# Kernel tuning notes

Hardware: AMD Instinct MI355X
Metric: run time of the kernel (lower is better)

## Reference

```python
import jax, jax.numpy as jnp
from jax import lax
import numpy as np

EPSILON = 22.6  # Cech radius; ~mean pairwise distance of N(0,1) points in 256-d


def _betti1(x, eps):
    """Faithful port of compute_betti_number for one epsilon. x: (B,T,C)."""
    B, T, C = x.shape
    # pairwise squared distances; compare d2 < eps^2 == (dist < eps), avoids sqrt
    sq = jnp.sum(x * x, axis=-1)                                  # (B,T)
    d2 = sq[:, :, None] + sq[:, None, :] - 2.0 * jnp.einsum('btc,bsc->bts', x, x)
    adj = d2 < (eps * eps)                                        # (B,T,T) bool; diagonal True (dist 0 < eps), matching torch
    adj = lax.stop_gradient(adj)                                  # original detaches x before topology
    # original: n_edges = np.sum(adjacency) // 2, diagonal included
    n_edges = jnp.sum(adj, axis=(1, 2)).astype(jnp.int32) // 2    # (B,)
    # connected components via min-label propagation + pointer jumping
    labels0 = jnp.broadcast_to(jnp.arange(T, dtype=jnp.int32), (B, T))

    def cond(state):
        return state[1]

    def body(state):
        labels, _ = state
        # min label among neighbors (diag True includes self)
        prop = jnp.min(jnp.where(adj, labels[:, None, :], T), axis=2).astype(jnp.int32)
        new = jnp.minimum(labels, prop)
        new = jnp.take_along_axis(new, new, axis=1)               # pointer jump -> O(log) convergence
        return new, jnp.any(new != labels)

    labels, _ = lax.while_loop(cond, body, (labels0, jnp.array(True)))
    # converged label = min index in component -> count roots
    n_comp = jnp.sum(labels == jnp.arange(T, dtype=jnp.int32)[None, :], axis=1).astype(jnp.int32)
    betti1 = jnp.maximum(0, n_edges - T + n_comp)                 # max(0, E - V + C)
    return betti1


def reference(x_before, x_after):
    betti_before = _betti1(x_before, EPSILON)
    betti_after = _betti1(x_after, EPSILON)
    diff = betti_after.astype(jnp.float32) - betti_before.astype(jnp.float32)
    return jnp.mean(diff * diff)


def setup_inputs() -> dict:
    key = jax.random.key(0)
    k1, k2 = jax.random.split(key)
    B, T, C = 4, 4096, 256
    x_before = jax.random.normal(k1, (B, T, C), dtype=jnp.float32)
    x_after = jax.random.normal(k2, (B, T, C), dtype=jnp.float32)
    return {"x_before": x_before, "x_after": x_after}
```

## Files before the change

kernel.cpp:

```cpp
#include <hip/hip_runtime.h>
#include <stdint.h>

#define TDIM 4096
#define CDIM 256
#define NMAT 8

typedef __attribute__((ext_vector_type(8))) __bf16 bf16x8;
typedef __attribute__((ext_vector_type(4))) float f32x4;

__device__ __forceinline__ unsigned short f2bf(float f) {
  unsigned int u = __float_as_uint(f);
  return (unsigned short)((u + 0x7FFFu + ((u >> 16) & 1u)) >> 16);
}
__device__ __forceinline__ void g2lds16(const void* g, void* l) {
  __builtin_amdgcn_global_load_lds((__attribute__((address_space(1))) void*)(void*)g,
                                   (__attribute__((address_space(3))) void*)l, 16, 0, 0);
}
__device__ __forceinline__ unsigned long long shfl_xor_u64(unsigned long long v, int m) {
  int lo = __shfl_xor((int)(unsigned int)(v & 0xFFFFFFFFull), m);
  int hi = __shfl_xor((int)(unsigned int)(v >> 32), m);
  return ((unsigned long long)(unsigned int)hi << 32) | (unsigned int)lo;
}

__global__ __launch_bounds__(256) void prep_kernel(
    const float* __restrict__ xb, const float* __restrict__ xa,
    unsigned short* __restrict__ xhi, float* __restrict__ sq) {
  const int wid = threadIdx.x >> 6, lane = threadIdx.x & 63;
  const int gr = blockIdx.x * 4 + wid;
  const int mb = gr >> 12;
  const size_t rowoff = (size_t)gr * CDIM;
  const float* src = (mb < 4) ? (xb + rowoff) : (xa + rowoff - (size_t)4 * TDIM * CDIM);

  float4 v = ((const float4*)src)[lane];
  float vv[4] = {v.x, v.y, v.z, v.w};
  unsigned short h[4];
  float ss = 0.f;
#pragma unroll
  for (int c = 0; c < 4; ++c) {
    h[c] = f2bf(vv[c]);
    ss += vv[c] * vv[c];
  }
  *(ushort4*)&xhi[rowoff + lane * 4] = make_ushort4(h[0], h[1], h[2], h[3]);
#pragma unroll
  for (int off = 32; off; off >>= 1) ss += __shfl_down(ss, off);
  if (lane == 0) sq[gr] = ss;
}

__global__ __launch_bounds__(256) void prep4_kernel(
    const float* __restrict__ src0, unsigned short* __restrict__ xhi,
    float* __restrict__ sq4) {
  const int wid = threadIdx.x >> 6, lane = threadIdx.x & 63;
  const int gr = blockIdx.x * 4 + wid;
  const size_t rowoff = (size_t)gr * CDIM;
  float4 v = ((const float4*)(src0 + rowoff))[lane];
  float vv[4] = {v.x, v.y, v.z, v.w};
  unsigned short h[4];
  float ss = 0.f;
#pragma unroll
  for (int c = 0; c < 4; ++c) {
    h[c] = f2bf(vv[c]);
    ss += vv[c] * vv[c];
  }
  *(ushort4*)&xhi[rowoff + lane * 4] = make_ushort4(h[0], h[1], h[2], h[3]);
#pragma unroll
  for (int off = 32; off; off >>= 1) ss += __shfl_down(ss, off);
  if (lane == 0) sq4[gr] = ss;
}

__global__ __launch_bounds__(256, 3) void gram_kernel(
    const unsigned short* __restrict__ xhi, const float* __restrict__ sq,
    unsigned long long* __restrict__ adj, unsigned int* __restrict__ edgepart,
    int ep_base, int mb_base, int mbits) {
  __shared__ unsigned short As[128 * 64];
  __shared__ unsigned short Bs[128 * 64];
  __shared__ unsigned int wcnt[4];

  const int tid = threadIdx.x;
  const int wid = tid >> 6, lane = tid & 63;
  const int wr = wid >> 1, wc = wid & 1;

  const int mbl = blockIdx.x & ((1 << mbits) - 1);
  const int mb = mb_base + mbl;
  int rem = blockIdx.x >> mbits;
  int ti = 0;
  while (rem >= 32 - ti) { rem -= 32 - ti; ++ti; }
  const int tj = ti + rem;

  const unsigned short* hi = xhi + (size_t)mbl * TDIM * CDIM;
  const float* sqm = sq + (size_t)mb * TDIM;

  f32x4 acc[4][4] = {};

  const int ldrow = (lane >> 3);
  const int ldcol = ((lane & 7) ^ ldrow) * 8;

  for (int ks = 0; ks < 4; ++ks) {
    const int kcol = ks * 64;
    __syncthreads();
#pragma unroll
    for (int i = 0; i < 4; ++i) {
      const int chunk = wid * 4 + i;
      const int row = chunk * 8 + ldrow;
      g2lds16(hi + (size_t)(ti * 128 + row) * CDIM + kcol + ldcol, &As[chunk * 512]);
      g2lds16(hi + (size_t)(tj * 128 + row) * CDIM + kcol + ldcol, &Bs[chunk * 512]);
    }
    asm volatile("s_waitcnt vmcnt(0)" ::: "memory");
    __syncthreads();
#pragma unroll
    for (int kk = 0; kk < 2; ++kk) {
      bf16x8 a[4], b[4];
      const int hi16 = lane >> 4;
#pragma unroll
      for (int m = 0; m < 4; ++m) {
        const int row = wr * 64 + m * 16 + (lane & 15);
        a[m] = *(const bf16x8*)&As[row * 64 + (((kk * 4 + hi16) ^ (row & 7)) * 8)];
      }
#pragma unroll
      for (int n = 0; n < 4; ++n) {
        const int row = wc * 64 + n * 16 + (lane & 15);
        b[n] = *(const bf16x8*)&Bs[row * 64 + (((kk * 4 + hi16) ^ (row & 7)) * 8)];
      }
#pragma unroll
      for (int m = 0; m < 4; ++m)
#pragma unroll
        for (int n = 0; n < 4; ++n)
          acc[m][n] = __builtin_amdgcn_mfma_f32_16x16x32_bf16(a[m], b[n], acc[m][n], 0, 0, 0);
    }
  }

  const float EPS2 = (float)(22.6 * 22.6);
  unsigned long long* adjm = adj + (size_t)mb * TDIM * 64;
  const int gt = (lane >> 2) & 3;
  const int mtgt = lane >> 4, rtgt = lane & 3;
  unsigned long long vrow = 0;

  float4 srv[4];
#pragma unroll
  for (int m = 0; m < 4; ++m)
    srv[m] = *(const float4*)&sqm[ti * 128 + wr * 64 + m * 16 + (lane >> 4) * 4];
  float scv[4];
#pragma unroll
  for (int n = 0; n < 4; ++n) scv[n] = sqm[tj * 128 + wc * 64 + n * 16 + (lane & 15)];

#pragma unroll
  for (int m = 0; m < 4; ++m) {
#pragma unroll
    for (int r = 0; r < 4; ++r) {
      const float srr = ((const float*)&srv[m])[r];
      unsigned long long bl[4];
#pragma unroll
      for (int n = 0; n < 4; ++n) {
        const float d2 = srr + scv[n] - 2.0f * acc[m][n][r];
        bl[n] = __ballot(d2 < EPS2);
      }
      if (m == mtgt && r == rtgt)
        vrow = ((bl[0] >> (16 * gt)) & 0xFFFFULL)         | (((bl[1] >> (16 * gt)) & 0xFFFFULL) << 16) |
               (((bl[2] >> (16 * gt)) & 0xFFFFULL) << 32) | (((bl[3] >> (16 * gt)) & 0xFFFFULL) << 48);
    }
  }
  adjm[(size_t)(ti * 128 + wr * 64 + lane) * 64 + tj * 2 + wc] = vrow;

  {
    unsigned int pc = (unsigned int)__popcll(vrow);
#pragma unroll
    for (int off = 32; off; off >>= 1) pc += __shfl_down(pc, off);
    if (lane == 0) wcnt[wid] = (ti != tj) ? pc * 2u : pc;
  }

  if (ti != tj) {
    const unsigned long long mk[6] = {
        0x5555555555555555ull, 0x3333333333333333ull, 0x0F0F0F0F0F0F0F0Full,
        0x00FF00FF00FF00FFull, 0x0000FFFF0000FFFFull, 0x00000000FFFFFFFFull};
#pragma unroll
    for (int s = 0; s < 6; ++s) {
      const int d = 1 << s;
      const unsigned long long m = mk[s];
      unsigned long long t = shfl_xor_u64(vrow, d);
      if ((lane & d) == 0) vrow = (vrow & m) | ((t & m) << d);
      else                 vrow = (vrow & ~m) | ((t & ~m) >> d);
    }
    adjm[(size_t)(tj * 128 + wc * 64 + lane) * 64 + ti * 2 + wr] = vrow;
  }

  __syncthreads();
  if (tid == 0)
    edgepart[ep_base + blockIdx.x] = wcnt[0] + wcnt[1] + wcnt[2] + wcnt[3];
}

__global__ __launch_bounds__(1024) void cc_iter_kernel(const unsigned long long* __restrict__ adj,
                                                       int* __restrict__ ncomp) {
  __shared__ int lab[TDIM];
  __shared__ int nxt[TDIM];
  __shared__ int changed;
  __shared__ int croots;
  const int mb = blockIdx.x;
  const unsigned long long* A = adj + (size_t)mb * TDIM * 64;
  const int tid = threadIdx.x;

  for (int i = tid; i < TDIM; i += 1024) {
    unsigned long long w0 = A[(size_t)i * 64];
    nxt[i] = w0 ? (__ffsll(w0) - 1) : i;
  }
  __syncthreads();
  for (int i = tid; i < TDIM; i += 1024) lab[i] = nxt[nxt[i]];
  __syncthreads();

  for (int it = 0; it < 96; ++it) {
    if (tid == 0) changed = 0;
    __syncthreads();
    for (int i = tid; i < TDIM; i += 1024) {
      const int cur = lab[i];
      int mn = cur;
      if (cur > 0) {
        for (int wd = 0; wd < 64 && mn > 0; ++wd) {
          unsigned long long w = A[(size_t)i * 64 + wd];
          while (w && mn > 0) {
            const int bit = __ffsll(w) - 1;
            w &= w - 1;
            mn = min(mn, lab[wd * 64 + bit]);
          }
        }
        if (mn < cur) changed = 1;
      }
      nxt[i] = mn;
    }
    __syncthreads();
    const int ch = changed;
    for (int i = tid; i < TDIM; i += 1024) lab[i] = nxt[nxt[i]];
    __syncthreads();
    if (!ch) break;
  }

  if (tid == 0) croots = 0;
  __syncthreads();
  int c = 0;
  for (int i = tid; i < TDIM; i += 1024) c += (lab[i] == i);
  atomicAdd(&croots, c);
  __syncthreads();
  if (tid == 0) ncomp[mb] = croots;
}

__global__ __launch_bounds__(512) void final_kernel(const unsigned int* __restrict__ edgepart,
                                                    const int* __restrict__ ncomp,
                                                    float* __restrict__ out, int big) {
  __shared__ unsigned long long es[8];
  const int wid = threadIdx.x >> 6, lane = threadIdx.x & 63;
  unsigned long long s = 0;
  if (big) {
    for (int k = lane; k < 528; k += 64) s += edgepart[k * 8 + wid];
  } else {
    const int base = (wid < 4) ? 0 : 2112;
    const int m4 = wid & 3;
    for (int k = lane; k < 528; k += 64) s += edgepart[base + k * 4 + m4];
  }
#pragma unroll
  for (int off = 32; off; off >>= 1) s += __shfl_down(s, off);
  if (lane == 0) es[wid] = s;
  __syncthreads();
  if (threadIdx.x == 0) {
    double acc = 0.0;
    for (int b = 0; b < 4; ++b) {
      long long e0 = (long long)(es[b] >> 1);
      long long bet0 = e0 - TDIM + (long long)ncomp[b];
      if (bet0 < 0) bet0 = 0;
      long long e1 = (long long)(es[4 + b] >> 1);
      long long bet1 = e1 - TDIM + (long long)ncomp[4 + b];
      if (bet1 < 0) bet1 = 0;
      double d = (double)(bet1 - bet0);
      acc += d * d;
    }
    out[0] = (float)(acc * 0.25);
  }
}

extern "C" void kernel_launch(void* const* d_in, const int* in_sizes, int n_in,
                              void* d_out, int out_size, void* d_ws, size_t ws_size,
                              hipStream_t stream) {
  (void)in_sizes; (void)n_in; (void)out_size;
  const float* xb = (const float*)d_in[0];
  const float* xa = (const float*)d_in[1];
  char* ws = (char*)d_ws;

  const bool big = (ws_size == 0) || (ws_size >= ((size_t)34 << 20));

  if (big) {
    const size_t XHI_OFF = 0;
    const size_t ADJ_OFF = (size_t)NMAT * TDIM * CDIM * 2;
    const size_t SQ_OFF  = ADJ_OFF + (size_t)NMAT * TDIM * 64 * 8;
    const size_t NC_OFF  = SQ_OFF + (size_t)NMAT * TDIM * 4;
    const size_t EDGE_OFF = NC_OFF + 64;

    unsigned short* xhi = (unsigned short*)(ws + XHI_OFF);
    unsigned long long* adj = (unsigned long long*)(ws + ADJ_OFF);
    float* sq = (float*)(ws + SQ_OFF);
    int* ncomp = (int*)(ws + NC_OFF);
    unsigned int* edgepart = (unsigned int*)(ws + EDGE_OFF);

    prep_kernel<<<NMAT * TDIM / 4, 256, 0, stream>>>(xb, xa, xhi, sq);
    gram_kernel<<<NMAT * 528, 256, 0, stream>>>(xhi, sq, adj, edgepart, 0, 0, 3);
    cc_iter_kernel<<<NMAT, 1024, 0, stream>>>(adj, ncomp);
    final_kernel<<<1, 512, 0, stream>>>(edgepart, ncomp, (float*)d_out, 1);
  } else {
    const size_t XHI_OFF = 0;
    const size_t ADJ_OFF = (size_t)4 * TDIM * CDIM * 2;
    const size_t SQ_OFF  = ADJ_OFF + (size_t)NMAT * TDIM * 64 * 8;
    const size_t NC_OFF  = SQ_OFF + (size_t)NMAT * TDIM * 4;
    const size_t EDGE_OFF = NC_OFF + 64;

    unsigned short* xhi = (unsigned short*)(ws + XHI_OFF);
    unsigned long long* adj = (unsigned long long*)(ws + ADJ_OFF);
    float* sq = (float*)(ws + SQ_OFF);
    int* ncomp = (int*)(ws + NC_OFF);
    unsigned int* edgepart = (unsigned int*)(ws + EDGE_OFF);

    prep4_kernel<<<TDIM, 256, 0, stream>>>(xb, xhi, sq);
    gram_kernel<<<4 * 528, 256, 0, stream>>>(xhi, sq, adj, edgepart, 0, 0, 2);
    prep4_kernel<<<TDIM, 256, 0, stream>>>(xa, xhi, sq + (size_t)4 * TDIM);
    gram_kernel<<<4 * 528, 256, 0, stream>>>(xhi, sq, adj, edgepart, 2112, 4, 2);
    cc_iter_kernel<<<NMAT, 1024, 0, stream>>>(adj, ncomp);
    final_kernel<<<1, 512, 0, stream>>>(edgepart, ncomp, (float*)d_out, 0);
  }
}
```

Measured before the change: 81.13 us.

## Compute two column tiles per gram block to reuse the A tile

Each gram block now processes a row tile against two adjacent column tiles (tj0, tj0+1), sharing the A tile loaded into LDS and the A fragments across twice as many MFMAs. The upper-triangle pair enumeration shrinks from 528 to 272 blocks per matrix, and the edge-count reduction and offsets are adjusted to match. The aim is to cut redundant global and LDS loads of A and per-block overhead. In exchange it doubles the accumulator registers, which lowers the occupancy hint from 3 to 2, adds LDS use, and leaves some blocks at the end of each row with a single tile doing redundant loads.

```diff
diff --git a/kernel.cpp b/kernel.cpp
--- a/kernel.cpp
+++ b/kernel.cpp
@@ -4,6 +4,7 @@
 #define TDIM 4096
 #define CDIM 256
 #define NMAT 8
+#define NPAIR 272
 
 typedef __attribute__((ext_vector_type(8))) __bf16 bf16x8;
 typedef __attribute__((ext_vector_type(4))) float f32x4;
@@ -67,12 +68,12 @@
   if (lane == 0) sq4[gr] = ss;
 }
 
-__global__ __launch_bounds__(256, 3) void gram_kernel(
+__global__ __launch_bounds__(256, 2) void gram_kernel(
     const unsigned short* __restrict__ xhi, const float* __restrict__ sq,
     unsigned long long* __restrict__ adj, unsigned int* __restrict__ edgepart,
     int ep_base, int mb_base, int mbits) {
   __shared__ unsigned short As[128 * 64];
-  __shared__ unsigned short Bs[128 * 64];
+  __shared__ unsigned short Bs[2][128 * 64];
   __shared__ unsigned int wcnt[4];
 
   const int tid = threadIdx.x;
@@ -83,13 +84,15 @@
   const int mb = mb_base + mbl;
   int rem = blockIdx.x >> mbits;
   int ti = 0;
-  while (rem >= 32 - ti) { rem -= 32 - ti; ++ti; }
-  const int tj = ti + rem;
+  while (rem >= ((33 - ti) >> 1)) { rem -= (33 - ti) >> 1; ++ti; }
+  const int tj0 = ti + 2 * rem;
+  const int hasT1 = (tj0 < 31);
+  const int tj1 = hasT1 ? tj0 + 1 : tj0;
 
   const unsigned short* hi = xhi + (size_t)mbl * TDIM * CDIM;
   const float* sqm = sq + (size_t)mb * TDIM;
 
-  f32x4 acc[4][4] = {};
+  f32x4 acc[2][4][4] = {};
 
   const int ldrow = (lane >> 3);
   const int ldcol = ((lane & 7) ^ ldrow) * 8;
@@ -102,13 +105,14 @@
       const int chunk = wid * 4 + i;
       const int row = chunk * 8 + ldrow;
       g2lds16(hi + (size_t)(ti * 128 + row) * CDIM + kcol + ldcol, &As[chunk * 512]);
-      g2lds16(hi + (size_t)(tj * 128 + row) * CDIM + kcol + ldcol, &Bs[chunk * 512]);
+      g2lds16(hi + (size_t)(tj0 * 128 + row) * CDIM + kcol + ldcol, &Bs[0][chunk * 512]);
+      g2lds16(hi + (size_t)(tj1 * 128 + row) * CDIM + kcol + ldcol, &Bs[1][chunk * 512]);
     }
     asm volatile("s_waitcnt vmcnt(0)" ::: "memory");
     __syncthreads();
 #pragma unroll
     for (int kk = 0; kk < 2; ++kk) {
-      bf16x8 a[4], b[4];
+      bf16x8 a[4], b[2][4];
       const int hi16 = lane >> 4;
 #pragma unroll
       for (int m = 0; m < 4; ++m) {
@@ -118,13 +122,17 @@
 #pragma unroll
       for (int n = 0; n < 4; ++n) {
         const int row = wc * 64 + n * 16 + (lane & 15);
-        b[n] = *(const bf16x8*)&Bs[row * 64 + (((kk * 4 + hi16) ^ (row & 7)) * 8)];
+        const int off = row * 64 + (((kk * 4 + hi16) ^ (row & 7)) * 8);
+        b[0][n] = *(const bf16x8*)&Bs[0][off];
+        b[1][n] = *(const bf16x8*)&Bs[1][off];
       }
 #pragma unroll
       for (int m = 0; m < 4; ++m)
 #pragma unroll
-        for (int n = 0; n < 4; ++n)
-          acc[m][n] = __builtin_amdgcn_mfma_f32_16x16x32_bf16(a[m], b[n], acc[m][n], 0, 0, 0);
+        for (int n = 0; n < 4; ++n) {
+          acc[0][m][n] = __builtin_amdgcn_mfma_f32_16x16x32_bf16(a[m], b[0][n], acc[0][m][n], 0, 0, 0);
+          acc[1][m][n] = __builtin_amdgcn_mfma_f32_16x16x32_bf16(a[m], b[1][n], acc[1][m][n], 0, 0, 0);
+        }
     }
   }
 
@@ -132,55 +140,66 @@
   unsigned long long* adjm = adj + (size_t)mb * TDIM * 64;
   const int gt = (lane >> 2) & 3;
   const int mtgt = lane >> 4, rtgt = lane & 3;
-  unsigned long long vrow = 0;
 
   float4 srv[4];
 #pragma unroll
   for (int m = 0; m < 4; ++m)
     srv[m] = *(const float4*)&sqm[ti * 128 + wr * 64 + m * 16 + (lane >> 4) * 4];
-  float scv[4];
-#pragma unroll
-  for (int n = 0; n < 4; ++n) scv[n] = sqm[tj * 128 + wc * 64 + n * 16 + (lane & 15)];
-
-#pragma unroll
-  for (int m = 0; m < 4; ++m) {
-#pragma unroll
-    for (int r = 0; r < 4; ++r) {
-      const float srr = ((const float*)&srv[m])[r];
-      unsigned long long bl[4];
-#pragma unroll
-      for (int n = 0; n < 4; ++n) {
-        const float d2 = srr + scv[n] - 2.0f * acc[m][n][r];
-        bl[n] = __ballot(d2 < EPS2);
-      }
-      if (m == mtgt && r == rtgt)
-        vrow = ((bl[0] >> (16 * gt)) & 0xFFFFULL)         | (((bl[1] >> (16 * gt)) & 0xFFFFULL) << 16) |
-               (((bl[2] >> (16 * gt)) & 0xFFFFULL) << 32) | (((bl[3] >> (16 * gt)) & 0xFFFFULL) << 48);
-    }
-  }
-  adjm[(size_t)(ti * 128 + wr * 64 + lane) * 64 + tj * 2 + wc] = vrow;
-
-  {
-    unsigned int pc = (unsigned int)__popcll(vrow);
-#pragma unroll
-    for (int off = 32; off; off >>= 1) pc += __shfl_down(pc, off);
-    if (lane == 0) wcnt[wid] = (ti != tj) ? pc * 2u : pc;
-  }
-
-  if (ti != tj) {
-    const unsigned long long mk[6] = {
-        0x5555555555555555ull, 0x3333333333333333ull, 0x0F0F0F0F0F0F0F0Full,
-        0x00FF00FF00FF00FFull, 0x0000FFFF0000FFFFull, 0x00000000FFFFFFFFull};
-#pragma unroll
-    for (int s = 0; s < 6; ++s) {
-      const int d = 1 << s;
-      const unsigned long long m = mk[s];
-      unsigned long long t = shfl_xor_u64(vrow, d);
-      if ((lane & d) == 0) vrow = (vrow & m) | ((t & m) << d);
-      else                 vrow = (vrow & ~m) | ((t & ~m) >> d);
-    }
-    adjm[(size_t)(tj * 128 + wc * 64 + lane) * 64 + ti * 2 + wr] = vrow;
-  }
+  float scv[2][4];
+#pragma unroll
+  for (int n = 0; n < 4; ++n) {
+    scv[0][n] = sqm[tj0 * 128 + wc * 64 + n * 16 + (lane & 15)];
+    scv[1][n] = sqm[tj1 * 128 + wc * 64 + n * 16 + (lane & 15)];
+  }
+
+  unsigned int myc = 0;
+#pragma unroll
+  for (int t = 0; t < 2; ++t) {
+    if (t == 0 || hasT1) {
+      const int tjt = t ? tj1 : tj0;
+      unsigned long long vrow = 0;
+#pragma unroll
+      for (int m = 0; m < 4; ++m) {
+#pragma unroll
+        for (int r = 0; r < 4; ++r) {
+          const float srr = ((const float*)&srv[m])[r];
+          unsigned long long bl[4];
+#pragma unroll
+          for (int n = 0; n < 4; ++n) {
+            const float d2 = srr + scv[t][n] - 2.0f * acc[t][m][n][r];
+            bl[n] = __ballot(d2 < EPS2);
+          }
+          if (m == mtgt && r == rtgt)
+            vrow = ((bl[0] >> (16 * gt)) & 0xFFFFULL)         | (((bl[1] >> (16 * gt)) & 0xFFFFULL) << 16) |
+                   (((bl[2] >> (16 * gt)) & 0xFFFFULL) << 32) | (((bl[3] >> (16 * gt)) & 0xFFFFULL) << 48);
+        }
+      }
+      adjm[(size_t)(ti * 128 + wr * 64 + lane) * 64 + tjt * 2 + wc] = vrow;
+
+      {
+        unsigned int pc = (unsigned int)__popcll(vrow);
+#pragma unroll
+        for (int off = 32; off; off >>= 1) pc += __shfl_down(pc, off);
+        if (lane == 0) myc += (ti != tjt) ? pc * 2u : pc;
+      }
+
+      if (ti != tjt) {
+        const unsigned long long mk[6] = {
+            0x5555555555555555ull, 0x3333333333333333ull, 0x0F0F0F0F0F0F0F0Full,
+            0x00FF00FF00FF00FFull, 0x0000FFFF0000FFFFull, 0x00000000FFFFFFFFull};
+#pragma unroll
+        for (int s = 0; s < 6; ++s) {
+          const int d = 1 << s;
+          const unsigned long long mkk = mk[s];
+          unsigned long long tt = shfl_xor_u64(vrow, d);
+          if ((lane & d) == 0) vrow = (vrow & mkk) | ((tt & mkk) << d);
+          else                 vrow = (vrow & ~mkk) | ((tt & ~mkk) >> d);
+        }
+        adjm[(size_t)(tjt * 128 + wc * 64 + lane) * 64 + ti * 2 + wr] = vrow;
+      }
+    }
+  }
+  if (lane == 0) wcnt[wid] = myc;
 
   __syncthreads();
   if (tid == 0)
@@ -247,11 +266,11 @@
   const int wid = threadIdx.x >> 6, lane = threadIdx.x & 63;
   unsigned long long s = 0;
   if (big) {
-    for (int k = lane; k < 528; k += 64) s += edgepart[k * 8 + wid];
+    for (int k = lane; k < NPAIR; k += 64) s += edgepart[k * 8 + wid];
   } else {
-    const int base = (wid < 4) ? 0 : 2112;
+    const int base = (wid < 4) ? 0 : 4 * NPAIR;
     const int m4 = wid & 3;
-    for (int k = lane; k < 528; k += 64) s += edgepart[base + k * 4 + m4];
+    for (int k = lane; k < NPAIR; k += 64) s += edgepart[base + k * 4 + m4];
   }
 #pragma unroll
   for (int off = 32; off; off >>= 1) s += __shfl_down(s, off);
@@ -297,7 +316,7 @@
     unsigned int* edgepart = (unsigned int*)(ws + EDGE_OFF);
 
     prep_kernel<<<NMAT * TDIM / 4, 256, 0, stream>>>(xb, xa, xhi, sq);
-    gram_kernel<<<NMAT * 528, 256, 0, stream>>>(xhi, sq, adj, edgepart, 0, 0, 3);
+    gram_kernel<<<NMAT * NPAIR, 256, 0, stream>>>(xhi, sq, adj, edgepart, 0, 0, 3);
     cc_iter_kernel<<<NMAT, 1024, 0, stream>>>(adj, ncomp);
     final_kernel<<<1, 512, 0, stream>>>(edgepart, ncomp, (float*)d_out, 1);
   } else {
@@ -314,9 +333,9 @@
     unsigned int* edgepart = (unsigned int*)(ws + EDGE_OFF);
 
     prep4_kernel<<<TDIM, 256, 0, stream>>>(xb, xhi, sq);
-    gram_kernel<<<4 * 528, 256, 0, stream>>>(xhi, sq, adj, edgepart, 0, 0, 2);
+    gram_kernel<<<4 * NPAIR, 256, 0, stream>>>(xhi, sq, adj, edgepart, 0, 0, 2);
     prep4_kernel<<<TDIM, 256, 0, stream>>>(xa, xhi, sq + (size_t)4 * TDIM);
-    gram_kernel<<<4 * 528, 256, 0, stream>>>(xhi, sq, adj, edgepart, 2112, 4, 2);
+    gram_kernel<<<4 * NPAIR, 256, 0, stream>>>(xhi, sq, adj, edgepart, 4 * NPAIR, 4, 2);
     cc_iter_kernel<<<NMAT, 1024, 0, stream>>>(adj, ncomp);
     final_kernel<<<1, 512, 0, stream>>>(edgepart, ncomp, (float*)d_out, 0);
   }
```

New measurement: 80.70 us (median of 2 runs). About the same (-0.5%).
